# Kernel optimization log

Measured on AMD Instinct MI355X. Metric: run time of the kernel, lower is better.

The kernel has to match this reference:

```python
import jax, jax.numpy as jnp
import numpy as np

THRESH = 1.0
GAMA = 1.0
TAU0 = 0.5

# ZIF surrogate spike: forward hard step, backward triangular surrogate
@jax.custom_vjp
def zif(x):
    return (x > 0).astype(x.dtype)

def _zif_fwd(x):
    return zif(x), x

def _zif_bwd(x, g):
    surr = (1.0 / GAMA) * (1.0 / GAMA) * jnp.clip(GAMA - jnp.abs(x), 0.0, None)
    return (g * surr,)

zif.defvjp(_zif_fwd, _zif_bwd)


def setup_inputs() -> dict:
    key = jax.random.key(0)
    k1, k2, k3, k4, k5 = jax.random.split(key, 5)
    B, T, C, H, W = 32, 8, 128, 32, 32
    red = 4
    x = jax.random.normal(k1, (B, T, C, H, W), dtype=jnp.float32)
    # fc1: Linear(C, C//red); fc2: Linear(C//red, 1); PyTorch default init scale
    s1 = 1.0 / np.sqrt(C)
    s2 = 1.0 / np.sqrt(C // red)
    w1 = jax.random.uniform(k2, (C // red, C), jnp.float32, -s1, s1)
    b1 = jax.random.uniform(k3, (C // red,), jnp.float32, -s1, s1)
    w2 = jax.random.uniform(k4, (1, C // red), jnp.float32, -s2, s2)
    b2 = jax.random.uniform(k5, (1,), jnp.float32, -s2, s2)
    return {"x": x, "w1": w1, "b1": b1, "w2": w2, "b2": b2}


def reference(x, w1, b1, w2, b2):
    B, T, C, H, W = x.shape

    def step(carry, xt):
        mem, tau = carry  # mem: [B,C,H,W], tau: [B,1,1,1]
        mem = mem * tau + xt
        # SE-style gating MLP on channel means
        x_mean = jnp.mean(mem, axis=(-1, -2))          # [B,C]
        embed = jax.nn.relu(x_mean @ w1.T + b1)        # [B,C//r]
        lifp = jax.nn.sigmoid(embed @ w2.T + b2)       # [B,1]
        new_tau = lifp[:, :, None, None]               # [B,1,1,1]
        spike = zif(mem - THRESH)
        mem = (1.0 - spike) * mem
        return (mem, new_tau), spike

    mem0 = jnp.zeros((B, C, H, W), dtype=x.dtype)
    tau0 = jnp.full((B, 1, 1, 1), TAU0, dtype=x.dtype)
    xt = jnp.transpose(x, (1, 0, 2, 3, 4))  # [T,B,C,H,W]
    _, spikes = jax.lax.scan(step, (mem0, tau0), xt)
    return jnp.transpose(spikes, (1, 0, 2, 3, 4))  # [B,T,C,H,W]
```

## Files before the change

kernel.cpp:

```cpp
#include <hip/hip_runtime.h>

typedef float v4f __attribute__((ext_vector_type(4)));

#define NB   32
#define NT   8
#define NC   128
#define NQ   256
#define CRED 32

#define NWORDS (NT * NB * NC * 2)

__device__ unsigned long long g_xw[NWORDS];

__global__ __launch_bounds__(256)
void lif_init() {
    int i = threadIdx.x + blockIdx.x * blockDim.x;
    if (i < NWORDS) g_xw[i] = 0ull;
}

#define LDS_BARRIER() asm volatile("s_waitcnt lgkmcnt(0)\n\ts_barrier" ::: "memory")

__global__ __launch_bounds__(256, 4)
void dynamic_lif(const float* __restrict__ x,
                 const float* __restrict__ w1,
                 const float* __restrict__ b1,
                 const float* __restrict__ w2,
                 const float* __restrict__ b2,
                 float* __restrict__ out)
{
    const int bid = blockIdx.x;
    const int b   = bid >> 5;
    const int c0  = (bid & 31) << 2;
    const int tid = threadIdx.x;
    const int wv  = tid >> 6;
    const int ln  = tid & 63;

    __shared__ double       s_part[4][4];
    __shared__ unsigned int s_w[256];
    __shared__ float        s_tau;

    const v4f* __restrict__ x4 = (const v4f*)x;
    v4f* __restrict__ o4       = (v4f*)out;

    v4f mem[4];
    #pragma unroll
    for (int p = 0; p < 4; ++p) mem[p] = (v4f){0.f, 0.f, 0.f, 0.f};

    float tau = 0.5f;

    v4f xv[4];
    #pragma unroll
    for (int p = 0; p < 4; ++p)
        xv[p] = __builtin_nontemporal_load(x4 + ((b * NT + 0) * NC + c0 + p) * NQ + tid);

    for (int t = 0; t < NT; ++t) {
        double psum[4];
        #pragma unroll
        for (int p = 0; p < 4; ++p) {
            v4f m = mem[p];
            m.x = fmaf(m.x, tau, xv[p].x);
            m.y = fmaf(m.y, tau, xv[p].y);
            m.z = fmaf(m.z, tau, xv[p].z);
            m.w = fmaf(m.w, tau, xv[p].w);
            psum[p] = ((double)m.x + (double)m.y) + ((double)m.z + (double)m.w);
            mem[p] = m;
        }

        #pragma unroll
        for (int p = 0; p < 4; ++p) {
            double s = psum[p];
            #pragma unroll
            for (int off = 32; off > 0; off >>= 1) s += __shfl_down(s, off);
            if (ln == 0) s_part[p][wv] = s;
        }
        LDS_BARRIER();

        if (t == NT - 1) {
            #pragma unroll
            for (int p = 0; p < 4; ++p) {
                v4f m = mem[p];
                v4f sp;
                sp.x = (m.x > 1.0f) ? 1.0f : 0.0f;
                sp.y = (m.y > 1.0f) ? 1.0f : 0.0f;
                sp.z = (m.z > 1.0f) ? 1.0f : 0.0f;
                sp.w = (m.w > 1.0f) ? 1.0f : 0.0f;
                __builtin_nontemporal_store(sp,
                    o4 + ((b * NT + t) * NC + c0 + p) * NQ + tid);
            }
            break;
        }

        if (tid < 4) {
            double s = (s_part[tid][0] + s_part[tid][1]) +
                       (s_part[tid][2] + s_part[tid][3]);
            double mean = s * (1.0 / 1024.0);
            unsigned long long bits = __double_as_longlong(mean);
            unsigned long long tag  = ((unsigned long long)(t + 1)) << 32;
            const int base = ((t * NB + b) * NC + c0 + tid) * 2;
            __hip_atomic_store(&g_xw[base + 0], tag | (bits & 0xffffffffull),
                               __ATOMIC_RELAXED, __HIP_MEMORY_SCOPE_AGENT);
            __hip_atomic_store(&g_xw[base + 1], tag | (bits >> 32),
                               __ATOMIC_RELAXED, __HIP_MEMORY_SCOPE_AGENT);
        }

        #pragma unroll
        for (int p = 0; p < 4; ++p)
            xv[p] = __builtin_nontemporal_load(
                x4 + ((b * NT + (t + 1)) * NC + c0 + p) * NQ + tid);

        {
            const int idx = ((t * NB + b) * NC + (tid >> 1)) * 2 + (tid & 1);
            const unsigned int want = (unsigned int)(t + 1);
            unsigned long long w;
            for (;;) {
                w = __hip_atomic_load(&g_xw[idx], __ATOMIC_RELAXED,
                                      __HIP_MEMORY_SCOPE_AGENT);
                if ((unsigned int)(w >> 32) == want) break;
                __builtin_amdgcn_s_sleep(1);
            }
            s_w[tid] = (unsigned int)w;
        }
        asm volatile("" ::: "memory");

        #pragma unroll
        for (int p = 0; p < 4; ++p) {
            v4f m = mem[p];
            v4f sp;
            sp.x = (m.x > 1.0f) ? 1.0f : 0.0f;
            sp.y = (m.y > 1.0f) ? 1.0f : 0.0f;
            sp.z = (m.z > 1.0f) ? 1.0f : 0.0f;
            sp.w = (m.w > 1.0f) ? 1.0f : 0.0f;
            __builtin_nontemporal_store(sp, o4 + ((b * NT + t) * NC + c0 + p) * NQ + tid);
            m.x = (m.x > 1.0f) ? 0.0f : m.x;
            m.y = (m.y > 1.0f) ? 0.0f : m.y;
            m.z = (m.z > 1.0f) ? 0.0f : m.z;
            m.w = (m.w > 1.0f) ? 0.0f : m.w;
            mem[p] = m;
        }

        LDS_BARRIER();

        double e = 0.0;
        if (tid < CRED) {
            const v4f* __restrict__ w1v = (const v4f*)(w1 + tid * NC);
            double acc = (double)b1[tid];
            #pragma unroll
            for (int q = 0; q < NC / 4; ++q) {
                v4f wq = w1v[q];
                #pragma unroll
                for (int k = 0; k < 4; ++k) {
                    const int c = 4 * q + k;
                    unsigned long long bits =
                        ((unsigned long long)s_w[2 * c + 1] << 32) | s_w[2 * c];
                    double xm = __longlong_as_double(bits);
                    acc += xm * (double)((k == 0) ? wq.x : (k == 1) ? wq.y
                                         : (k == 2) ? wq.z : wq.w);
                }
            }
            double emb = acc > 0.0 ? acc : 0.0;
            e = emb * (double)w2[tid];
        }
        #pragma unroll
        for (int off = 32; off > 0; off >>= 1) e += __shfl_down(e, off);
        if (tid == 0) {
            double z = e + (double)b2[0];
            s_tau = (float)(1.0 / (1.0 + exp(-z)));
        }
        LDS_BARRIER();
        tau = s_tau;
    }
}

extern "C" void kernel_launch(void* const* d_in, const int* in_sizes, int n_in,
                              void* d_out, int out_size, void* d_ws, size_t ws_size,
                              hipStream_t stream) {
    const float* x  = (const float*)d_in[0];
    const float* w1 = (const float*)d_in[1];
    const float* b1 = (const float*)d_in[2];
    const float* w2 = (const float*)d_in[3];
    const float* b2 = (const float*)d_in[4];
    float* out      = (float*)d_out;

    hipLaunchKernelGGL(lif_init, dim3((NWORDS + 255) / 256), dim3(256),
                       0, stream);
    hipLaunchKernelGGL(dynamic_lif, dim3(NB * NC / 4), dim3(256), 0, stream,
                       x, w1, b1, w2, b2, out);
}
```

Baseline: 292.6 us.

## Widen blocks to 16 channels and issue spike stores before cross-block wait

```diff
diff --git a/kernel.cpp b/kernel.cpp
--- a/kernel.cpp
+++ b/kernel.cpp
@@ -7,6 +7,7 @@
 #define NC   128
 #define NQ   256
 #define CRED 32
+#define CPB  16
 
 #define NWORDS (NT * NB * NC * 2)
 
@@ -20,7 +21,7 @@
 
 #define LDS_BARRIER() asm volatile("s_waitcnt lgkmcnt(0)\n\ts_barrier" ::: "memory")
 
-__global__ __launch_bounds__(256, 4)
+__global__ __launch_bounds__(1024, 4)
 void dynamic_lif(const float* __restrict__ x,
                  const float* __restrict__ w1,
                  const float* __restrict__ b1,
@@ -29,18 +30,22 @@
                  float* __restrict__ out)
 {
     const int bid = blockIdx.x;
-    const int b   = bid >> 5;
-    const int c0  = (bid & 31) << 2;
+    const int b   = bid >> 3;
+    const int c0  = (bid & 7) << 4;
     const int tid = threadIdx.x;
-    const int wv  = tid >> 6;
+    const int sub = tid >> 8;
+    const int q   = tid & 255;
+    const int wig = (tid >> 6) & 3;
     const int ln  = tid & 63;
 
-    __shared__ double       s_part[4][4];
+    __shared__ double       s_part[CPB][4];
     __shared__ unsigned int s_w[256];
     __shared__ float        s_tau;
 
     const v4f* __restrict__ x4 = (const v4f*)x;
     v4f* __restrict__ o4       = (v4f*)out;
+
+    const int cbase = c0 + (sub << 2);
 
     v4f mem[4];
     #pragma unroll
@@ -51,7 +56,7 @@
     v4f xv[4];
     #pragma unroll
     for (int p = 0; p < 4; ++p)
-        xv[p] = __builtin_nontemporal_load(x4 + ((b * NT + 0) * NC + c0 + p) * NQ + tid);
+        xv[p] = __builtin_nontemporal_load(x4 + ((b * NT + 0) * NC + cbase + p) * NQ + q);
 
     for (int t = 0; t < NT; ++t) {
         double psum[4];
@@ -71,7 +76,7 @@
             double s = psum[p];
             #pragma unroll
             for (int off = 32; off > 0; off >>= 1) s += __shfl_down(s, off);
-            if (ln == 0) s_part[p][wv] = s;
+            if (ln == 0) s_part[(sub << 2) + p][wig] = s;
         }
         LDS_BARRIER();
 
@@ -85,12 +90,12 @@
                 sp.z = (m.z > 1.0f) ? 1.0f : 0.0f;
                 sp.w = (m.w > 1.0f) ? 1.0f : 0.0f;
                 __builtin_nontemporal_store(sp,
-                    o4 + ((b * NT + t) * NC + c0 + p) * NQ + tid);
+                    o4 + ((b * NT + t) * NC + cbase + p) * NQ + q);
             }
             break;
         }
 
-        if (tid < 4) {
+        if (tid < CPB) {
             double s = (s_part[tid][0] + s_part[tid][1]) +
                        (s_part[tid][2] + s_part[tid][3]);
             double mean = s * (1.0 / 1024.0);
@@ -106,10 +111,26 @@
         #pragma unroll
         for (int p = 0; p < 4; ++p)
             xv[p] = __builtin_nontemporal_load(
-                x4 + ((b * NT + (t + 1)) * NC + c0 + p) * NQ + tid);
+                x4 + ((b * NT + (t + 1)) * NC + cbase + p) * NQ + q);
+        #pragma unroll
+        for (int p = 0; p < 4; ++p) {
+            v4f m = mem[p];
+            v4f sp;
+            sp.x = (m.x > 1.0f) ? 1.0f : 0.0f;
+            sp.y = (m.y > 1.0f) ? 1.0f : 0.0f;
+            sp.z = (m.z > 1.0f) ? 1.0f : 0.0f;
+            sp.w = (m.w > 1.0f) ? 1.0f : 0.0f;
+            __builtin_nontemporal_store(sp,
+                o4 + ((b * NT + t) * NC + cbase + p) * NQ + q);
+            m.x = (m.x > 1.0f) ? 0.0f : m.x;
+            m.y = (m.y > 1.0f) ? 0.0f : m.y;
+            m.z = (m.z > 1.0f) ? 0.0f : m.z;
+            m.w = (m.w > 1.0f) ? 0.0f : m.w;
+            mem[p] = m;
+        }
 
-        {
-            const int idx = ((t * NB + b) * NC + (tid >> 1)) * 2 + (tid & 1);
+        if (tid < 256) {
+            const int idx = (t * NB + b) * NC * 2 + tid;
             const unsigned int want = (unsigned int)(t + 1);
             unsigned long long w;
             for (;;) {
@@ -120,24 +141,6 @@
             }
             s_w[tid] = (unsigned int)w;
         }
-        asm volatile("" ::: "memory");
-
-        #pragma unroll
-        for (int p = 0; p < 4; ++p) {
-            v4f m = mem[p];
-            v4f sp;
-            sp.x = (m.x > 1.0f) ? 1.0f : 0.0f;
-            sp.y = (m.y > 1.0f) ? 1.0f : 0.0f;
-            sp.z = (m.z > 1.0f) ? 1.0f : 0.0f;
-            sp.w = (m.w > 1.0f) ? 1.0f : 0.0f;
-            __builtin_nontemporal_store(sp, o4 + ((b * NT + t) * NC + c0 + p) * NQ + tid);
-            m.x = (m.x > 1.0f) ? 0.0f : m.x;
-            m.y = (m.y > 1.0f) ? 0.0f : m.y;
-            m.z = (m.z > 1.0f) ? 0.0f : m.z;
-            m.w = (m.w > 1.0f) ? 0.0f : m.w;
-            mem[p] = m;
-        }
-
         LDS_BARRIER();
 
         double e = 0.0;
@@ -145,11 +148,11 @@
             const v4f* __restrict__ w1v = (const v4f*)(w1 + tid * NC);
             double acc = (double)b1[tid];
             #pragma unroll
-            for (int q = 0; q < NC / 4; ++q) {
-                v4f wq = w1v[q];
+            for (int qq = 0; qq < NC / 4; ++qq) {
+                v4f wq = w1v[qq];
                 #pragma unroll
                 for (int k = 0; k < 4; ++k) {
-                    const int c = 4 * q + k;
+                    const int c = 4 * qq + k;
                     unsigned long long bits =
                         ((unsigned long long)s_w[2 * c + 1] << 32) | s_w[2 * c];
                     double xm = __longlong_as_double(bits);
@@ -183,6 +186,6 @@
 
     hipLaunchKernelGGL(lif_init, dim3((NWORDS + 255) / 256), dim3(256),
                        0, stream);
-    hipLaunchKernelGGL(dynamic_lif, dim3(NB * NC / 4), dim3(256), 0, stream,
+    hipLaunchKernelGGL(dynamic_lif, dim3(NB * NC / CPB), dim3(1024), 0, stream,
                        x, w1, b1, w2, b2, out);
 }
```

After: 268.3 us. 8.3% less time.
